# Optimization experiments

Measured on AMD Instinct MI355X. Metric: run time of the kernel, lower is better.

## Reference

```python
import jax, jax.numpy as jnp
import numpy as np

N_HEAD = 16


def setup_inputs() -> dict:
    key = jax.random.key(0)
    ks = jax.random.split(key, 6)
    B, T, C = 2, 2048, 1024
    hs = C // N_HEAD  # 64
    block_minus_1 = 2048  # block_size - 1
    x = jax.random.normal(ks[0], (B, T, C), dtype=jnp.float32)
    W1 = jax.random.normal(ks[1], (C, C), dtype=jnp.float32) * (1.0 / np.sqrt(C))
    b1 = jnp.zeros((C,), dtype=jnp.float32)
    # original init: uniform(-1e-3, 1e-3)
    w2 = jax.random.uniform(ks[2], (hs, block_minus_1), dtype=jnp.float32, minval=-1e-3, maxval=1e-3)
    b2 = jnp.zeros((block_minus_1,), dtype=jnp.float32)
    Wv = jax.random.normal(ks[3], (C, C), dtype=jnp.float32) * (1.0 / np.sqrt(C))
    bv = jnp.zeros((C,), dtype=jnp.float32)
    Wp = jax.random.normal(ks[4], (C, C), dtype=jnp.float32) * (1.0 / np.sqrt(C))
    bp = jnp.zeros((C,), dtype=jnp.float32)
    return {"x": x, "W1": W1, "b1": b1, "w2": w2, "b2": b2,
            "Wv": Wv, "bv": bv, "Wp": Wp, "bp": bp}


def reference(x, W1, b1, w2, b2, Wv, bv, Wp, bp):
    B, T, C = x.shape
    hs = C // N_HEAD
    r = jax.nn.relu(x @ W1.T + b1).reshape(B, T, N_HEAD, hs).transpose(0, 2, 1, 3)
    # synthesizer scores: (B, nh, T, T) = relu_out @ w2[:, :T] + b2[:T]
    att = jnp.einsum('bhtd,dj->bhtj', r, w2[:, :T]) + b2[:T]
    causal = jnp.tril(jnp.ones((T, T), dtype=bool))
    att = jnp.where(causal[None, None], att, jnp.float32(-1e10))
    att = jax.nn.softmax(att, axis=-1)  # attn_drop = 0 (eval)
    v = (x @ Wv.T + bv).reshape(B, T, N_HEAD, hs).transpose(0, 2, 1, 3)
    y = jnp.einsum('bhtj,bhjd->bhtd', att, v)
    y = y.transpose(0, 2, 1, 3).reshape(B, T, C)
    return y @ Wp.T + bp  # resid_drop = 0 (eval)
```

## Files before the change

### kernel.cpp

```cpp
#include <hip/hip_runtime.h>

typedef __bf16 bf16x8 __attribute__((ext_vector_type(8)));
typedef float f32x4 __attribute__((ext_vector_type(4)));

__device__ __forceinline__ unsigned short f2bf(float f) {
  union { float f; unsigned u; } v; v.f = f;
  unsigned u = v.u;
  return (unsigned short)((u + 0x7fffu + ((u >> 16) & 1u)) >> 16);
}
__device__ __forceinline__ unsigned short f2bf_fast(float f) {
  union { float f; unsigned u; } v; v.f = f;
  return (unsigned short)((v.u + 0x8000u) >> 16);
}
__device__ __forceinline__ void gload_lds16(const void* g, void* l) {
  __builtin_amdgcn_global_load_lds(
      (const __attribute__((address_space(1))) unsigned int*)g,
      (__attribute__((address_space(3))) unsigned int*)l, 16, 0, 0);
}
__device__ __forceinline__ void cvt4(const float* __restrict__ s,
                                     unsigned short* __restrict__ d, int u) {
  f32x4 v = ((const f32x4*)s)[u];
  union { unsigned short s[4]; unsigned long long u; } o;
  o.s[0] = f2bf(v[0]); o.s[1] = f2bf(v[1]); o.s[2] = f2bf(v[2]); o.s[3] = f2bf(v[3]);
  ((unsigned long long*)d)[u] = o.u;
}


__global__ void prep(const float* __restrict__ x, const float* __restrict__ W1,
                     const float* __restrict__ Wv, const float* __restrict__ Wp,
                     const float* __restrict__ w2, const float* __restrict__ b2,
                     unsigned short* __restrict__ xb, unsigned short* __restrict__ W1b,
                     unsigned short* __restrict__ Wvb, unsigned short* __restrict__ Wpb,
                     unsigned short* __restrict__ w2t, unsigned short* __restrict__ ebj) {
  int u = blockIdx.x * 256 + threadIdx.x;
  if (u < 1048576) { cvt4(x, xb, u); return; }
  u -= 1048576;
  if (u < 262144) { cvt4(W1, W1b, u); return; }
  u -= 262144;
  if (u < 262144) { cvt4(Wv, Wvb, u); return; }
  u -= 262144;
  if (u < 262144) { cvt4(Wp, Wpb, u); return; }
  u -= 262144;
  if (u < 32768) {
    int j = u >> 4, d4 = (u & 15) * 4;
    union { unsigned short s[4]; unsigned long long x; } o;
#pragma unroll
    for (int i = 0; i < 4; ++i) o.s[i] = f2bf(w2[(d4 + i) * 2048 + j]);
    ((unsigned long long*)w2t)[u] = o.x;
    return;
  }
  u -= 32768;
  union { unsigned short s[4]; unsigned long long x; } o;
#pragma unroll
  for (int i = 0; i < 4; ++i) o.s[i] = f2bf(__expf(b2[u * 4 + i]));
  ((unsigned long long*)ebj)[u] = o.x;
}

__global__ __launch_bounds__(256) void gemm_rv(
    const unsigned short* __restrict__ xb, const unsigned short* __restrict__ W1b,
    const unsigned short* __restrict__ Wvb, const float* __restrict__ b1,
    const float* __restrict__ bv, const float* __restrict__ b2,
    unsigned short* __restrict__ rb, unsigned short* __restrict__ vtb) {
  __shared__ unsigned short Xs[128 * 64];
  __shared__ unsigned short W1s[64 * 64];
  __shared__ unsigned short Wvs[64 * 64];
  const int tm = blockIdx.x * 128, n0 = blockIdx.y * 64;
  const int tid = threadIdx.x;
  const int wv = tid >> 6, ln = tid & 63;
  const int quad = ln >> 4, lq = ln & 15;
  const int rowL = ln >> 3;
  const int kc = (((ln & 7) ^ rowL) & 7) * 8;
  const int sx = lq & 7;
  const int ko0 = (quad ^ sx) * 8, ko1 = ((4 + quad) ^ sx) * 8;

  f32x4 accR[2][4];
  f32x4 accV[8];
  const f32x4 zf = {0.f, 0.f, 0.f, 0.f};
#pragma unroll
  for (int i = 0; i < 2; ++i)
#pragma unroll
    for (int j = 0; j < 4; ++j) accR[i][j] = zf;
#pragma unroll
  for (int j = 0; j < 8; ++j) accV[j] = zf;

  for (int k0 = 0; k0 < 1024; k0 += 64) {
    __syncthreads();
#pragma unroll
    for (int l = 0; l < 4; ++l) {
      int row = l * 32 + wv * 8 + rowL;
      gload_lds16(xb + (tm + row) * 1024 + k0 + kc, &Xs[l * 2048 + wv * 512]);
    }
#pragma unroll
    for (int l = 0; l < 2; ++l) {
      int row = l * 32 + wv * 8 + rowL;
      gload_lds16(W1b + (n0 + row) * 1024 + k0 + kc, &W1s[l * 2048 + wv * 512]);
      gload_lds16(Wvb + (n0 + row) * 1024 + k0 + kc, &Wvs[l * 2048 + wv * 512]);
    }
    __syncthreads();
#pragma unroll
    for (int kk = 0; kk < 2; ++kk) {
      const int ko = kk ? ko1 : ko0;
      bf16x8 xa[2], w1f[4];
#pragma unroll
      for (int mi = 0; mi < 2; ++mi)
        xa[mi] = *(const bf16x8*)&Xs[(wv * 32 + mi * 16 + lq) * 64 + ko];
#pragma unroll
      for (int ni = 0; ni < 4; ++ni)
        w1f[ni] = *(const bf16x8*)&W1s[(ni * 16 + lq) * 64 + ko];
#pragma unroll
      for (int mi = 0; mi < 2; ++mi)
#pragma unroll
        for (int ni = 0; ni < 4; ++ni)
          accR[mi][ni] = __builtin_amdgcn_mfma_f32_16x16x32_bf16(xa[mi], w1f[ni], accR[mi][ni], 0, 0, 0);
      bf16x8 wva = *(const bf16x8*)&Wvs[(wv * 16 + lq) * 64 + ko];
#pragma unroll
      for (int nj = 0; nj < 8; ++nj) {
        bf16x8 xbf = *(const bf16x8*)&Xs[(nj * 16 + lq) * 64 + ko];
        accV[nj] = __builtin_amdgcn_mfma_f32_16x16x32_bf16(wva, xbf, accV[nj], 0, 0, 0);
      }
    }
  }
#pragma unroll
  for (int ni = 0; ni < 4; ++ni) {
    int col = n0 + ni * 16 + lq;
    float bc = b1[col];
#pragma unroll
    for (int mi = 0; mi < 2; ++mi)
#pragma unroll
      for (int rg = 0; rg < 4; ++rg) {
        int row = tm + wv * 32 + mi * 16 + quad * 4 + rg;
        float v = accR[mi][ni][rg] + bc;
        rb[row * 1024 + col] = f2bf(v > 0.f ? v : 0.f);
      }
  }
#pragma unroll
  for (int nj = 0; nj < 8; ++nj) {
    int tok = tm + nj * 16 + lq;
    float eb = __expf(b2[tok & 2047]);
#pragma unroll
    for (int rg = 0; rg < 4; ++rg) {
      int ch = n0 + wv * 16 + quad * 4 + rg;
      vtb[ch * 4096 + tok] = f2bf((accV[nj][rg] + bv[ch]) * eb);
    }
  }
}

__global__ __launch_bounds__(256) void gemm_p(
    const unsigned short* __restrict__ A, const unsigned short* __restrict__ Bt,
    const float* __restrict__ bias, float* __restrict__ C) {
  __shared__ unsigned short As[64 * 64];
  __shared__ unsigned short Bs[64 * 64];
  const int tid = threadIdx.x;
  const int wv = tid >> 6, ln = tid & 63;
  const int quad = ln >> 4, lq = ln & 15;
  const int tileM = blockIdx.y * 64, tileN = blockIdx.x * 64;
  const int rowL = ln >> 3;
  const int kc = (((ln & 7) ^ rowL) & 7) * 8;
  const int sx = lq & 7;
  const int ko0 = (quad ^ sx) * 8, ko1 = ((4 + quad) ^ sx) * 8;

  f32x4 acc[4];
  const f32x4 zf = {0.f, 0.f, 0.f, 0.f};
#pragma unroll
  for (int j = 0; j < 4; ++j) acc[j] = zf;

  for (int k0 = 0; k0 < 1024; k0 += 64) {
    __syncthreads();
#pragma unroll
    for (int l = 0; l < 2; ++l) {
      int row = l * 32 + wv * 8 + rowL;
      gload_lds16(A + (tileM + row) * 1024 + k0 + kc, &As[l * 2048 + wv * 512]);
      gload_lds16(Bt + (tileN + row) * 1024 + k0 + kc, &Bs[l * 2048 + wv * 512]);
    }
    __syncthreads();
#pragma unroll
    for (int kk = 0; kk < 2; ++kk) {
      const int ko = kk ? ko1 : ko0;
      bf16x8 af = *(const bf16x8*)&As[(wv * 16 + lq) * 64 + ko];
#pragma unroll
      for (int ni = 0; ni < 4; ++ni) {
        bf16x8 bfr = *(const bf16x8*)&Bs[(ni * 16 + lq) * 64 + ko];
        acc[ni] = __builtin_amdgcn_mfma_f32_16x16x32_bf16(af, bfr, acc[ni], 0, 0, 0);
      }
    }
  }
#pragma unroll
  for (int ni = 0; ni < 4; ++ni) {
    int col = tileN + ni * 16 + lq;
#pragma unroll
    for (int rg = 0; rg < 4; ++rg) {
      int row = tileM + wv * 16 + quad * 4 + rg;
      C[row * 1024 + col] = acc[ni][rg] + bias[col];
    }
  }
}

__global__ __launch_bounds__(256, 2) void attn(
    const unsigned short* __restrict__ r, const unsigned short* __restrict__ w2t,
    const unsigned short* __restrict__ vt, const unsigned short* __restrict__ ebj,
    unsigned short* __restrict__ y) {
  __shared__ unsigned short W2s[2][64 * 64];
  __shared__ unsigned short Vs[2][64 * 64];
  __shared__ unsigned short Ps[4][16 * 64];

  const int tid = threadIdx.x;
  const int wv = tid >> 6, ln = tid & 63;
  const int quad = ln >> 4, lq = ln & 15;
  const int bh = blockIdx.x, b = bh >> 4, h = bh & 15;
  const int p = blockIdx.y;
  const int ta = p, tb = 31 - p;
  const int t0a = ta * 64, t0b = tb * 64;
  const int rowL = ln >> 3;
  const int kc = (((ln & 7) ^ rowL) & 7) * 8;
  const int sx = lq & 7;
  const int ko0 = (quad ^ sx) * 8, ko1 = ((4 + quad) ^ sx) * 8;

  bf16x8 ra[2][2];
  {
    const unsigned short* base = r + (b * 2048 + wv * 16 + lq) * 1024 + h * 64 + quad * 8;
    ra[0][0] = *(const bf16x8*)(base + t0a * 1024);
    ra[0][1] = *(const bf16x8*)(base + t0a * 1024 + 32);
    ra[1][0] = *(const bf16x8*)(base + t0b * 1024);
    ra[1][1] = *(const bf16x8*)(base + t0b * 1024 + 32);
  }

  f32x4 accY[4];
  f32x4 accL;
  const f32x4 zf = {0.f, 0.f, 0.f, 0.f};
#pragma unroll
  for (int nd = 0; nd < 4; ++nd) accY[nd] = zf;
  accL = zf;

  auto stage = [&](int jt, int bi) {
    int j0 = jt * 64;
#pragma unroll
    for (int l = 0; l < 2; ++l) {
      int row = l * 32 + wv * 8 + rowL;
      gload_lds16(w2t + (j0 + row) * 64 + kc, &W2s[bi][l * 2048 + wv * 512]);
      gload_lds16(vt + (h * 64 + row) * 4096 + b * 2048 + j0 + kc,
                  &Vs[bi][l * 2048 + wv * 512]);
    }
  };

  stage(0, 0);
  for (int it = 0; it <= 32; ++it) {
    const int cb = it & 1;
    __syncthreads();
    if (it < 32) {
      int nit = it + 1;
      int njt = (nit <= p) ? nit : (nit - p - 1);
      stage(njt, cb ^ 1);
    }
    const int s = (it <= p) ? 0 : 1;
    const int jt = (it <= p) ? it : (it - p - 1);
    const int tts = s ? tb : ta;
    const int t0 = tts * 64;
    const int j0 = jt * 64;

    bf16x8 eb0 = *(const bf16x8*)&ebj[j0 + quad * 8];
    bf16x8 eb1 = *(const bf16x8*)&ebj[j0 + 32 + quad * 8];
    bf16x8 w2f0[4], w2f1[4];
#pragma unroll
    for (int ni = 0; ni < 4; ++ni) {
      w2f0[ni] = *(const bf16x8*)&W2s[cb][(ni * 16 + lq) * 64 + ko0];
      w2f1[ni] = *(const bf16x8*)&W2s[cb][(ni * 16 + lq) * 64 + ko1];
    }

    f32x4 sv[4] = {zf, zf, zf, zf};
#pragma unroll
    for (int ni = 0; ni < 4; ++ni) {
      sv[ni] = __builtin_amdgcn_mfma_f32_16x16x32_bf16(ra[s][0], w2f0[ni], sv[ni], 0, 0, 0);
      sv[ni] = __builtin_amdgcn_mfma_f32_16x16x32_bf16(ra[s][1], w2f1[ni], sv[ni], 0, 0, 0);
    }

    const bool diag = (jt == tts);
#pragma unroll
    for (int ni = 0; ni < 4; ++ni) {
      int j = j0 + ni * 16 + lq;
#pragma unroll
      for (int rg = 0; rg < 4; ++rg) {
        float pe = __expf(sv[ni][rg]);
        if (diag) {
          int t = t0 + wv * 16 + quad * 4 + rg;
          pe = (j <= t) ? pe : 0.f;
        }
        Ps[wv][(quad * 4 + rg) * 64 +
               (((ni * 2 + (lq >> 3)) ^ ((quad * 4 + rg) & 7)) * 8) + (lq & 7)] = f2bf_fast(pe);
      }
    }

#pragma unroll
    for (int kk = 0; kk < 2; ++kk) {
      const int ko = kk ? ko1 : ko0;
      bf16x8 pa = *(const bf16x8*)&Ps[wv][lq * 64 + ko];
#pragma unroll
      for (int nd = 0; nd < 4; ++nd) {
        bf16x8 bb = *(const bf16x8*)&Vs[cb][(nd * 16 + lq) * 64 + ko];
        accY[nd] = __builtin_amdgcn_mfma_f32_16x16x32_bf16(pa, bb, accY[nd], 0, 0, 0);
      }
      accL = __builtin_amdgcn_mfma_f32_16x16x32_bf16(pa, kk ? eb1 : eb0, accL, 0, 0, 0);
    }

    if (it == p || it == 32) {
      float inv[4];
#pragma unroll
      for (int rg = 0; rg < 4; ++rg) inv[rg] = __builtin_amdgcn_rcpf(accL[rg]);
#pragma unroll
      for (int nd = 0; nd < 4; ++nd)
#pragma unroll
        for (int rg = 0; rg < 4; ++rg) {
          int t = t0 + wv * 16 + quad * 4 + rg;
          y[(b * 2048 + t) * 1024 + h * 64 + nd * 16 + lq] = f2bf(accY[nd][rg] * inv[rg]);
        }
#pragma unroll
      for (int nd = 0; nd < 4; ++nd) accY[nd] = zf;
      accL = zf;
    }
  }
}

extern "C" void kernel_launch(void* const* d_in, const int* in_sizes, int n_in,
                              void* d_out, int out_size, void* d_ws, size_t ws_size,
                              hipStream_t stream) {
  const float* x  = (const float*)d_in[0];
  const float* W1 = (const float*)d_in[1];
  const float* b1 = (const float*)d_in[2];
  const float* w2 = (const float*)d_in[3];
  const float* b2 = (const float*)d_in[4];
  const float* Wv = (const float*)d_in[5];
  const float* bv = (const float*)d_in[6];
  const float* Wp = (const float*)d_in[7];
  const float* bp = (const float*)d_in[8];

  unsigned short* ws  = (unsigned short*)d_ws;
  unsigned short* xb   = ws;
  unsigned short* W1b  = ws + 4194304;
  unsigned short* Wvb  = ws + 5242880;
  unsigned short* Wpb  = ws + 6291456;
  unsigned short* w2t  = ws + 7340032;
  unsigned short* rb   = ws + 7471104;
  unsigned short* vt   = ws + 11665408;
  unsigned short* yb   = ws + 15859712;
  unsigned short* ebjb = ws + 20054016;

  prep<<<7298, 256, 0, stream>>>(x, W1, Wv, Wp, w2, b2, xb, W1b, Wvb, Wpb, w2t, ebjb);
  gemm_rv<<<dim3(32, 16), 256, 0, stream>>>(xb, W1b, Wvb, b1, bv, b2, rb, vt);
  attn<<<dim3(32, 16), 256, 0, stream>>>(rb, w2t, vt, ebjb, yb);
  gemm_p<<<dim3(16, 64), 256, 0, stream>>>(yb, Wpb, bp, (float*)d_out);
}
```

Baseline: 182.4 us.

## Share W2/V tile loads between paired query tiles in causal attention

Each workgroup handles two query tiles (ta, tb). It now walks the key tiles once up to tb and processes both query tiles against each staged W2/V tile, instead of staging them separately in two sequential passes. This cuts global-to-LDS traffic and the number of barriers, at the cost of a second set of accumulators and more register pressure. The blockIdx.y to pair mapping is also reordered, presumably to change how long-running pairs are spread across the launch.

```diff
diff --git a/kernel.cpp b/kernel.cpp
--- a/kernel.cpp
+++ b/kernel.cpp
@@ -207,7 +207,8 @@
   const int wv = tid >> 6, ln = tid & 63;
   const int quad = ln >> 4, lq = ln & 15;
   const int bh = blockIdx.x, b = bh >> 4, h = bh & 15;
-  const int p = blockIdx.y;
+  const int q = blockIdx.y;
+  const int p = (q < 8) ? q : 23 - q;
   const int ta = p, tb = 31 - p;
   const int t0a = ta * 64, t0b = tb * 64;
   const int rowL = ln >> 3;
@@ -224,12 +225,15 @@
     ra[1][1] = *(const bf16x8*)(base + t0b * 1024 + 32);
   }
 
-  f32x4 accY[4];
-  f32x4 accL;
+  f32x4 accY[2][4];
+  f32x4 accL[2];
   const f32x4 zf = {0.f, 0.f, 0.f, 0.f};
 #pragma unroll
-  for (int nd = 0; nd < 4; ++nd) accY[nd] = zf;
-  accL = zf;
+  for (int s = 0; s < 2; ++s) {
+    accL[s] = zf;
+#pragma unroll
+    for (int nd = 0; nd < 4; ++nd) accY[s][nd] = zf;
+  }
 
   auto stage = [&](int jt, int bi) {
     int j0 = jt * 64;
@@ -242,19 +246,55 @@
     }
   };
 
+#define TILE(S, T0, TT)                                                         \
+    {                                                                           \
+      f32x4 sv[4] = {zf, zf, zf, zf};                                           \
+      _Pragma("unroll") for (int ni = 0; ni < 4; ++ni) {                        \
+        sv[ni] = __builtin_amdgcn_mfma_f32_16x16x32_bf16(ra[S][0], w2f0[ni], sv[ni], 0, 0, 0); \
+        sv[ni] = __builtin_amdgcn_mfma_f32_16x16x32_bf16(ra[S][1], w2f1[ni], sv[ni], 0, 0, 0); \
+      }                                                                         \
+      const bool diag = (jt == (TT));                                           \
+      _Pragma("unroll") for (int ni = 0; ni < 4; ++ni) {                        \
+        int j = j0 + ni * 16 + lq;                                              \
+        _Pragma("unroll") for (int rg = 0; rg < 4; ++rg) {                      \
+          float pe = __expf(sv[ni][rg]);                                        \
+          if (diag) {                                                           \
+            int t = (T0) + wv * 16 + quad * 4 + rg;                             \
+            pe = (j <= t) ? pe : 0.f;                                           \
+          }                                                                     \
+          Ps[wv][(quad * 4 + rg) * 64 +                                         \
+                 (((ni * 2 + (lq >> 3)) ^ ((quad * 4 + rg) & 7)) * 8) + (lq & 7)] = f2bf_fast(pe); \
+        }                                                                       \
+      }                                                                         \
+      _Pragma("unroll") for (int kk = 0; kk < 2; ++kk) {                        \
+        const int ko = kk ? ko1 : ko0;                                          \
+        bf16x8 pa = *(const bf16x8*)&Ps[wv][lq * 64 + ko];                      \
+        _Pragma("unroll") for (int nd = 0; nd < 4; ++nd) {                      \
+          bf16x8 bb = *(const bf16x8*)&Vs[cb][(nd * 16 + lq) * 64 + ko];        \
+          accY[S][nd] = __builtin_amdgcn_mfma_f32_16x16x32_bf16(pa, bb, accY[S][nd], 0, 0, 0); \
+        }                                                                       \
+        accL[S] = __builtin_amdgcn_mfma_f32_16x16x32_bf16(pa, kk ? eb1 : eb0, accL[S], 0, 0, 0); \
+      }                                                                         \
+    }
+
+#define WRITEOUT(S, T0)                                                         \
+    {                                                                           \
+      float inv[4];                                                             \
+      _Pragma("unroll") for (int rg = 0; rg < 4; ++rg)                          \
+        inv[rg] = __builtin_amdgcn_rcpf(accL[S][rg]);                           \
+      _Pragma("unroll") for (int nd = 0; nd < 4; ++nd)                          \
+        _Pragma("unroll") for (int rg = 0; rg < 4; ++rg) {                      \
+          int t = (T0) + wv * 16 + quad * 4 + rg;                               \
+          y[(b * 2048 + t) * 1024 + h * 64 + nd * 16 + lq] =                    \
+              f2bf(accY[S][nd][rg] * inv[rg]);                                  \
+        }                                                                       \
+    }
+
   stage(0, 0);
-  for (int it = 0; it <= 32; ++it) {
-    const int cb = it & 1;
-    __syncthreads();
-    if (it < 32) {
-      int nit = it + 1;
-      int njt = (nit <= p) ? nit : (nit - p - 1);
-      stage(njt, cb ^ 1);
-    }
-    const int s = (it <= p) ? 0 : 1;
-    const int jt = (it <= p) ? it : (it - p - 1);
-    const int tts = s ? tb : ta;
-    const int t0 = tts * 64;
+  for (int jt = 0; jt <= tb; ++jt) {
+    const int cb = jt & 1;
+    __syncthreads();
+    if (jt < tb) stage(jt + 1, cb ^ 1);
     const int j0 = jt * 64;
 
     bf16x8 eb0 = *(const bf16x8*)&ebj[j0 + quad * 8];
@@ -266,57 +306,13 @@
       w2f1[ni] = *(const bf16x8*)&W2s[cb][(ni * 16 + lq) * 64 + ko1];
     }
 
-    f32x4 sv[4] = {zf, zf, zf, zf};
-#pragma unroll
-    for (int ni = 0; ni < 4; ++ni) {
-      sv[ni] = __builtin_amdgcn_mfma_f32_16x16x32_bf16(ra[s][0], w2f0[ni], sv[ni], 0, 0, 0);
-      sv[ni] = __builtin_amdgcn_mfma_f32_16x16x32_bf16(ra[s][1], w2f1[ni], sv[ni], 0, 0, 0);
-    }
-
-    const bool diag = (jt == tts);
-#pragma unroll
-    for (int ni = 0; ni < 4; ++ni) {
-      int j = j0 + ni * 16 + lq;
-#pragma unroll
-      for (int rg = 0; rg < 4; ++rg) {
-        float pe = __expf(sv[ni][rg]);
-        if (diag) {
-          int t = t0 + wv * 16 + quad * 4 + rg;
-          pe = (j <= t) ? pe : 0.f;
-        }
-        Ps[wv][(quad * 4 + rg) * 64 +
-               (((ni * 2 + (lq >> 3)) ^ ((quad * 4 + rg) & 7)) * 8) + (lq & 7)] = f2bf_fast(pe);
-      }
-    }
-
-#pragma unroll
-    for (int kk = 0; kk < 2; ++kk) {
-      const int ko = kk ? ko1 : ko0;
-      bf16x8 pa = *(const bf16x8*)&Ps[wv][lq * 64 + ko];
-#pragma unroll
-      for (int nd = 0; nd < 4; ++nd) {
-        bf16x8 bb = *(const bf16x8*)&Vs[cb][(nd * 16 + lq) * 64 + ko];
-        accY[nd] = __builtin_amdgcn_mfma_f32_16x16x32_bf16(pa, bb, accY[nd], 0, 0, 0);
-      }
-      accL = __builtin_amdgcn_mfma_f32_16x16x32_bf16(pa, kk ? eb1 : eb0, accL, 0, 0, 0);
-    }
-
-    if (it == p || it == 32) {
-      float inv[4];
-#pragma unroll
-      for (int rg = 0; rg < 4; ++rg) inv[rg] = __builtin_amdgcn_rcpf(accL[rg]);
-#pragma unroll
-      for (int nd = 0; nd < 4; ++nd)
-#pragma unroll
-        for (int rg = 0; rg < 4; ++rg) {
-          int t = t0 + wv * 16 + quad * 4 + rg;
-          y[(b * 2048 + t) * 1024 + h * 64 + nd * 16 + lq] = f2bf(accY[nd][rg] * inv[rg]);
-        }
-#pragma unroll
-      for (int nd = 0; nd < 4; ++nd) accY[nd] = zf;
-      accL = zf;
-    }
-  }
+    if (jt <= ta) TILE(0, t0a, ta);
+    TILE(1, t0b, tb);
+    if (jt == ta) WRITEOUT(0, t0a);
+  }
+  WRITEOUT(1, t0b);
+#undef TILE
+#undef WRITEOUT
 }
 
 extern "C" void kernel_launch(void* const* d_in, const int* in_sizes, int n_in,
```

Measured after the change: 171.9 us. -5.8%, faster.
